# Performance work log

Measured on AMD Instinct MI355X. Metric: run time of the kernel, lower is better.

## Reference

```python
import jax, jax.numpy as jnp
import numpy as np


def lstm_cell(x, h, c, wih, whh, bih, bhh):
    # torch gate order: i, f, g, o
    g = x @ wih.T + bih + h @ whh.T + bhh
    i, f, gg, o = jnp.split(g, 4, axis=-1)
    c = jax.nn.sigmoid(f) * c + jax.nn.sigmoid(i) * jnp.tanh(gg)
    h = jax.nn.sigmoid(o) * jnp.tanh(c)
    return h, c


def lstm_layer(xs, h0, c0, wih, whh, bih, bhh):
    # xs: [T, B, in]
    def step(carry, x_t):
        h, c = lstm_cell(x_t, carry[0], carry[1], wih, whh, bih, bhh)
        return (h, c), h
    (h, c), hs = jax.lax.scan(step, (h0, c0), xs)
    return hs, h, c


def setup_inputs() -> dict:
    key = jax.random.key(0)
    B, T, H, IN = 256, 512, 512, 1
    ks = jax.random.split(key, 32)
    r = lambda k, shape: (jax.random.normal(k, shape, dtype=jnp.float32) * 0.05)
    inp = {
        "x": jax.random.normal(ks[0], (B, T, IN), dtype=jnp.float32),
        "future": 64,
        # main LSTM (2 layers)
        "w_ih0": r(ks[1], (4 * H, IN)), "w_hh0": r(ks[2], (4 * H, H)),
        "b_ih0": r(ks[3], (4 * H,)),   "b_hh0": r(ks[4], (4 * H,)),
        "w_ih1": r(ks[5], (4 * H, H)), "w_hh1": r(ks[6], (4 * H, H)),
        "b_ih1": r(ks[7], (4 * H,)),   "b_hh1": r(ks[8], (4 * H,)),
        "fc_w": r(ks[9], (1, H)),      "fc_b": r(ks[10], (1,)),
        # prediction LSTM (2 layers) + its head
        "pw_ih0": r(ks[11], (4 * H, 1)), "pw_hh0": r(ks[12], (4 * H, H)),
        "pb_ih0": r(ks[13], (4 * H,)),   "pb_hh0": r(ks[14], (4 * H,)),
        "pw_ih1": r(ks[15], (4 * H, H)), "pw_hh1": r(ks[16], (4 * H, H)),
        "pb_ih1": r(ks[17], (4 * H,)),   "pb_hh1": r(ks[18], (4 * H,)),
        "pfc_w": r(ks[19], (1, H)),      "pfc_b": r(ks[20], (1,)),
    }
    return inp


def reference(x, future, w_ih0, w_hh0, b_ih0, b_hh0, w_ih1, w_hh1, b_ih1, b_hh1,
              fc_w, fc_b, pw_ih0, pw_hh0, pb_ih0, pb_hh0, pw_ih1, pw_hh1,
              pb_ih1, pb_hh1, pfc_w, pfc_b):
    B = x.shape[0]
    H = w_hh0.shape[1]
    z = jnp.zeros((B, H), dtype=jnp.float32)
    xs = jnp.swapaxes(x, 0, 1)  # [T, B, 1]
    # warmup pass over the observed sequence (inference: dropout inactive)
    hs0, h0, c0 = lstm_layer(xs, z, z, w_ih0, w_hh0, b_ih0, b_hh0)
    hs1, h1, c1 = lstm_layer(hs0, z, z, w_ih1, w_hh1, b_ih1, b_hh1)
    out = hs1[-1] @ fc_w.T + fc_b  # [B, 1]

    def pstep(carry, _):
        o, h0, c0, h1, c1 = carry
        h0, c0 = lstm_cell(o, h0, c0, pw_ih0, pw_hh0, pb_ih0, pb_hh0)
        h1, c1 = lstm_cell(h0, h1, c1, pw_ih1, pw_hh1, pb_ih1, pb_hh1)
        o = h1 @ pfc_w.T + pfc_b
        return (o, h0, c0, h1, c1), o

    _, outs = jax.lax.scan(pstep, (out, h0, c0, h1, c1), None, length=future - 1)
    all_outs = jnp.concatenate([out[None], outs], axis=0)  # [future, B, 1]
    return jnp.swapaxes(all_outs[..., 0], 0, 1)  # [B, future]
```

## Files before the change

### kernel.cpp

```cpp
#include <hip/hip_runtime.h>
#include <hip/hip_bf16.h>

#define TT  512
#define BB  256
#define HH  512
#define FUT 64
#define NBLK 128


struct Hdr { int dtflag; };

typedef __attribute__((ext_vector_type(8))) short short8;
typedef __attribute__((ext_vector_type(4))) float floatx4;

#define OFF_FLG   4096
#define OFF_W     20480
#define WSZ       ((size_t)2048*512*2)
#define OFF_H0    (OFF_W + 6*WSZ)
#define HSZ       ((size_t)BB*HH*2)
#define OFF_H1    (OFF_H0 + 4*HSZ)
#define OFF_OA    (OFF_H1 + 2*HSZ)
#define OASZ      ((size_t)FUT*BB*4)
#define NEED_WS   (OFF_OA + OASZ)

#define SPIN_CAP  (1L << 22)

__device__ __forceinline__ float bf2f(short s) {
  unsigned u = ((unsigned)(unsigned short)s) << 16;
  return __builtin_bit_cast(float, u);
}
__device__ __forceinline__ short f2bf(float f) {
  unsigned u = __builtin_bit_cast(unsigned, f);
  u = u + 0x7FFFu + ((u >> 16) & 1u);
  return (short)(u >> 16);
}
__device__ __forceinline__ float ldf(const void* p, long i, int dt) {
  return dt ? ((const float*)p)[i] : bf2f(((const short*)p)[i]);
}
__device__ __forceinline__ short8 cohld16(const short* p) {
  short8 v;
  asm volatile("global_load_dwordx4 %0, %1, off sc0 sc1"
               : "=v"(v) : "v"(p));
  return v;
}
__device__ __forceinline__ void cohst16(short* p, short8 v) {
  asm volatile("global_store_dwordx4 %0, %1, off sc0 sc1"
               :: "v"(p), "v"(v) : "memory");
}
#define WAITV(N) do { asm volatile("s_waitcnt vmcnt(" #N ")" ::: "memory"); \
                      __builtin_amdgcn_sched_barrier(0); } while (0)

__global__ void beacon_kernel(float* dout, float v) {
  if (threadIdx.x == 0) dout[0] = v;
}

__global__ __launch_bounds__(256) void probe1_kernel(const void* w, Hdr* hdr) {
  const int tid = threadIdx.x;
  const short* s = (const short*)w;
  float mx = 0.f;
  #pragma unroll
  for (int i = 0; i < 16; ++i) {
    float v = fabsf(bf2f(s[tid * 16 + i]));
    if (!(v == v)) v = 1e30f;
    mx = fmaxf(mx, v);
  }
  #pragma unroll
  for (int off = 32; off > 0; off >>= 1) mx = fmaxf(mx, __shfl_down(mx, off));
  __shared__ float wmax[4];
  if ((tid & 63) == 0) wmax[tid >> 6] = mx;
  __syncthreads();
  if (tid == 0) {
    float m = fmaxf(fmaxf(wmax[0], wmax[1]), fmaxf(wmax[2], wmax[3]));
    hdr->dtflag = (m > 1000.f) ? 1 : 0;
  }
}

__global__ __launch_bounds__(256) void cvt_kernel(const void* src, short* dst,
                                                  const Hdr* hdr) {
  const int dt = hdr->dtflag;
  const long i = ((long)blockIdx.x * 256 + threadIdx.x);
  if (dt) {
    const float4 v = ((const float4*)src)[i];
    short4 o;
    o.x = f2bf(v.x); o.y = f2bf(v.y); o.z = f2bf(v.z); o.w = f2bf(v.w);
    ((short4*)dst)[i] = o;
  } else {
    ((short4*)dst)[i] = ((const short4*)src)[i];
  }
}

__global__ __launch_bounds__(512, 1) void lstm_persist(
    const void* __restrict__ x,
    const void* __restrict__ w_ih0, const void* __restrict__ b_ih0,
    const void* __restrict__ b_hh0, const void* __restrict__ b_ih1,
    const void* __restrict__ b_hh1, const void* __restrict__ fc_w,
    const void* __restrict__ fc_b,  const void* __restrict__ pw_ih0,
    const void* __restrict__ pb_ih0, const void* __restrict__ pb_hh0,
    const void* __restrict__ pb_ih1, const void* __restrict__ pb_hh1,
    const void* __restrict__ pfc_w, const void* __restrict__ pfc_b,
    const short* __restrict__ Whh0, const short* __restrict__ Wih1,
    const short* __restrict__ Whh1, const short* __restrict__ pWhh0,
    const short* __restrict__ pWih1, const short* __restrict__ pWhh1,
    short* H0R, short* H1R, float* oA, int* flg,
    const Hdr* __restrict__ hdr, float* __restrict__ dout)
{
  const int dt  = hdr->dtflag;
  const int tid = threadIdx.x;
  const int role = blockIdx.x & 1;
  const int bg   = (blockIdx.x >> 1) & 1;
  const int ug   = blockIdx.x >> 2;
  const int U0   = ug * 16;
  const int B0   = bg * 128;

  int* F     = flg + bg * 2048;
  int* pub0  = F;
  int* pub1  = F + 576;
  int* cons1 = F + 1152;
  int* opub  = F + 1728;

  __shared__ __align__(16) short Wl[2][64][64][8];
  __shared__ __align__(16) short hbuf[128][16];
  __shared__ float bs[64];
  __shared__ float wih[64];

  const int lane = tid & 63;
  const int wv   = tid >> 6;
  const int ln   = lane & 15;
  const int q    = lane >> 4;
  const int bl   = wv*16 + ln;
  const long abase = (long)(B0 + bl) * 512 + q*8;

  float cst[4] = {0.f, 0.f, 0.f, 0.f};
  float fwk[4] = {0.f, 0.f, 0.f, 0.f};

#define H0S(G) (H0R + (size_t)((G) & 3) * 131072)
#define H1S(G) (H1R + (size_t)((G) & 1) * 131072)

#define SPIN(COND)                                                           \
  { long guard_ = 0;                                                         \
    while (COND) {                                                           \
      __builtin_amdgcn_s_sleep(1);                                           \
      if (++guard_ > SPIN_CAP) break;                                        \
    } }
#define POLL(P, T)                                                           \
  SPIN(__hip_atomic_load((P), __ATOMIC_RELAXED,                              \
                         __HIP_MEMORY_SCOPE_SYSTEM) < (T))
#define FADD(P)                                                              \
  __hip_atomic_fetch_add((P), 1, __ATOMIC_RELAXED,                           \
                         __HIP_MEMORY_SCOPE_SYSTEM)

#define STAGE16(SLOT, WG)                                                    \
  for (int i = tid; i < 4096; i += 512) {                                    \
    const int ks_ = i & 63, r_ = i >> 6;                                     \
    const long gr = (long)((r_ & 3) * 512 + U0 + (r_ >> 2)) * 512 + ks_ * 8; \
    *(short8*)&Wl[SLOT][ks_][r_][0] = *(const short8*)((WG) + gr);           \
  }

#define BIAS16(B1, B2, WIHP)                                                 \
  if (tid < 64) {                                                            \
    const long j = (long)(tid & 3) * 512 + U0 + (tid >> 2);                  \
    bs[tid] = ldf((B1), j, dt) + ldf((B2), j, dt);                           \
    wih[tid] = (WIHP) ? ldf((const void*)(WIHP), j, dt) : 0.f;               \
  }

#define FWLOAD(FWP)                                                          \
  { _Pragma("unroll")                                                        \
    for (int mt = 0; mt < 4; ++mt)                                           \
      fwk[mt] = ldf((FWP), U0 + mt*4 + q, dt); }

#define ZACC(A)                                                              \
  _Pragma("unroll") for (int mt_ = 0; mt_ < 4; ++mt_)                        \
    A[mt_] = (floatx4){0.f, 0.f, 0.f, 0.f};

#define GSEG1N(AP, ACC)                                                      \
  { const short* ap_ = (AP) + abase;                                         \
    short8 abuf[2][8];                                                       \
    _Pragma("unroll")                                                        \
    for (int i = 0; i < 8; ++i) abuf[0][i] = cohld16(ap_ + i*32);            \
    _Pragma("unroll")                                                        \
    for (int g = 0; g < 2; ++g) {                                            \
      if (g == 0) {                                                          \
        _Pragma("unroll")                                                    \
        for (int i = 0; i < 8; ++i)                                          \
          abuf[1][i] = cohld16(ap_ + (8+i)*32);                              \
        WAITV(8);                                                            \
      } else { WAITV(0); }                                                   \
      _Pragma("unroll")                                                      \
      for (int kk = 0; kk < 8; ++kk) {                                       \
        const int kb = g*8 + kk;                                             \
        _Pragma("unroll")                                                    \
        for (int mt = 0; mt < 4; ++mt) {                                     \
          short8 wf = *(const short8*)&Wl[0][kb*4 + q][mt*16 + ln][0];       \
          ACC[mt] = __builtin_amdgcn_mfma_f32_16x16x32_bf16(                 \
              wf, abuf[g][kk], ACC[mt], 0, 0, 0);                            \
        }                                                                    \
      }                                                                      \
    } }

#define GSEG2N(AP0, AP1, ACC)                                                \
  { const short* p0_ = (AP0) + abase;                                        \
    const short* p1_ = (AP1) + abase;                                        \
    short8 abuf[2][8];                                                       \
    _Pragma("unroll")                                                        \
    for (int i = 0; i < 8; ++i) abuf[0][i] = cohld16(p0_ + i*32);            \
    _Pragma("unroll")                                                        \
    for (int g = 0; g < 4; ++g) {                                            \
      if (g < 3) {                                                           \
        const short* np_ = ((g+1)&1) ? p1_ : p0_;                            \
        const int nb_ = ((g+1)>>1)*8;                                        \
        _Pragma("unroll")                                                    \
        for (int i = 0; i < 8; ++i)                                          \
          abuf[(g+1)&1][i] = cohld16(np_ + (nb_+i)*32);                      \
        WAITV(8);                                                            \
      } else { WAITV(0); }                                                   \
      const int sg_ = g & 1;                                                 \
      const int kbb_ = (g >> 1) * 8;                                         \
      _Pragma("unroll")                                                      \
      for (int kk = 0; kk < 8; ++kk) {                                       \
        const int kb = kbb_ + kk;                                            \
        _Pragma("unroll")                                                    \
        for (int mt = 0; mt < 4; ++mt) {                                     \
          short8 wf = *(const short8*)&Wl[sg_][kb*4 + q][mt*16 + ln][0];     \
          ACC[mt] = __builtin_amdgcn_mfma_f32_16x16x32_bf16(                 \
              wf, abuf[g&1][kk], ACC[mt], 0, 0, 0);                          \
        }                                                                    \
      }                                                                      \
    } }

#define EPI16(ACC, MODE, TV, SVO, HOUT, OSLOT)                               \
  { float sv = 0.f;                                                          \
    if ((MODE) == 0)      sv = ldf(x, (long)(B0 + bl)*TT + (TV), dt);        \
    else if ((MODE) == 2) sv = (SVO);                                        \
    float po = 0.f;                                                          \
    _Pragma("unroll")                                                        \
    for (int mt = 0; mt < 4; ++mt) {                                         \
      const int u = mt*4 + q;                                                \
      float gi = ACC[mt][0] + bs[u*4+0];                                     \
      float gf = ACC[mt][1] + bs[u*4+1];                                     \
      float gg = ACC[mt][2] + bs[u*4+2];                                     \
      float go = ACC[mt][3] + bs[u*4+3];                                     \
      if ((MODE) != 1) {                                                     \
        gi += sv*wih[u*4+0]; gf += sv*wih[u*4+1];                            \
        gg += sv*wih[u*4+2]; go += sv*wih[u*4+3];                            \
      }                                                                      \
      const float I = 1.f/(1.f+expf(-gi));                                   \
      const float F = 1.f/(1.f+expf(-gf));                                   \
      const float G = tanhf(gg);                                             \
      const float O = 1.f/(1.f+expf(-go));                                   \
      const float cn = F*cst[mt] + I*G;                                      \
      cst[mt] = cn;                                                          \
      const short hb16 = f2bf(O * tanhf(cn));                                \
      hbuf[bl][u] = hb16;                                                    \
      if ((OSLOT) != (float*)0) po += fwk[mt] * bf2f(hb16);                  \
    }                                                                        \
    if ((OSLOT) != (float*)0) {                                              \
      po += __shfl_xor(po, 16); po += __shfl_xor(po, 32);                    \
      if (lane < 16) atomicAdd((float*)(OSLOT) + bl, po);                    \
    }                                                                        \
    __syncthreads();                                                         \
    if (tid < 256) {                                                         \
      const int b_ = tid >> 1, hf_ = tid & 1;                                \
      short8 hv8 = *(const short8*)&hbuf[b_][hf_*8];                         \
      cohst16((HOUT) + (long)(B0 + b_)*512 + U0 + hf_*8, hv8);               \
    }                                                                        \
    asm volatile("s_waitcnt vmcnt(0)" ::: "memory");                         \
    __syncthreads(); }

  if (role == 0) {
    STAGE16(0, Whh0);
    BIAS16(b_ih0, b_hh0, w_ih0);
  } else {
    STAGE16(0, Wih1); STAGE16(1, Whh1);
    BIAS16(b_ih1, b_hh1, (const void*)0);
    FWLOAD(fc_w);
  }
  const float fcb  = ldf(fc_b, 0, dt);
  const float pfcb = ldf(pfc_b, 0, dt);
  __syncthreads();

  if (role == 0) {
    for (int g = 0; g < TT; ++g) {
      if (tid == 0) {
        if (g > 0)  POLL(pub0 + g - 1, 32);
        if (g >= 4) POLL(cons1 + g - 4, 32);
      }
      __syncthreads();
      floatx4 a[4]; ZACC(a);
      GSEG1N(H0S(g-1), a);
      EPI16(a, 0, g, 0.f, H0S(g), (float*)0);
      if (tid == 0) FADD(pub0 + g);
    }
    STAGE16(0, pWhh0);
    BIAS16(pb_ih0, pb_hh0, pw_ih0);
    __syncthreads();
    for (int s = 1; s < FUT; ++s) {
      const int g = 511 + s;
      if (tid == 0) {
        POLL(pub0 + g - 1, 32);
        POLL(cons1 + g - 4, 32);
        POLL(opub + s - 1, 32);
      }
      __syncthreads();
      const float ob_ = (s == 1) ? fcb : pfcb;
      const float o_ = __hip_atomic_load(
          oA + (long)(s-1)*BB + B0 + bl,
          __ATOMIC_RELAXED, __HIP_MEMORY_SCOPE_SYSTEM) + ob_;
      if (ug == 0 && lane < 16)
        dout[(long)(B0 + bl)*FUT + (s-1)] = o_;
      floatx4 a[4]; ZACC(a);
      GSEG1N(H0S(g-1), a);
      EPI16(a, 2, 0, o_, H0S(g), (float*)0);
      if (tid == 0) FADD(pub0 + g);
    }
    if (tid == 0) POLL(opub + FUT - 1, 32);
    __syncthreads();
    if (ug == 0 && lane < 16) {
      const float o_ = __hip_atomic_load(
          oA + (long)(FUT-1)*BB + B0 + bl,
          __ATOMIC_RELAXED, __HIP_MEMORY_SCOPE_SYSTEM) + pfcb;
      dout[(long)(B0 + bl)*FUT + (FUT-1)] = o_;
    }
  } else {
    for (int g = 0; g < TT; ++g) {
      if (tid == 0) {
        POLL(pub0 + g, 32);
        if (g > 0) POLL(pub1 + g - 1, 32);
      }
      __syncthreads();
      floatx4 a[4]; ZACC(a);
      GSEG2N(H0S(g), H1S(g-1), a);
      __syncthreads();
      if (tid == 0) FADD(cons1 + g);
      float* os_ = (g == TT-1) ? (oA + B0) : (float*)0;
      EPI16(a, 1, 0, 0.f, H1S(g), os_);
      if (tid == 0) {
        FADD(pub1 + g);
        if (g == TT-1) FADD(opub + 0);
      }
    }
    STAGE16(0, pWih1); STAGE16(1, pWhh1);
    BIAS16(pb_ih1, pb_hh1, (const void*)0);
    FWLOAD(pfc_w);
    __syncthreads();
    for (int s = 1; s < FUT; ++s) {
      const int g = 511 + s;
      if (tid == 0) {
        POLL(pub0 + g, 32);
        POLL(pub1 + g - 1, 32);
      }
      __syncthreads();
      floatx4 a[4]; ZACC(a);
      GSEG2N(H0S(g), H1S(g-1), a);
      __syncthreads();
      if (tid == 0) FADD(cons1 + g);
      EPI16(a, 1, 0, 0.f, H1S(g), oA + (long)s*BB + B0);
      if (tid == 0) { FADD(pub1 + g); FADD(opub + s); }
    }
  }
#undef STAGE16
#undef BIAS16
#undef FWLOAD
#undef ZACC
#undef GSEG1N
#undef GSEG2N
#undef EPI16
#undef SPIN
#undef POLL
#undef FADD
#undef H0S
#undef H1S
}

extern "C" void kernel_launch(void* const* d_in, const int* in_sizes, int n_in,
                              void* d_out, int out_size, void* d_ws, size_t ws_size,
                              hipStream_t stream) {
  float* dout = (float*)d_out;

  static const int exp_sizes[22] = {
    131072, 1, 2048, 1048576, 2048, 2048, 1048576, 1048576, 2048, 2048,
    512, 1, 2048, 1048576, 2048, 2048, 1048576, 1048576, 2048, 2048, 512, 1};
  int code = -1, m = 0;
  if (n_in != 22) { code = 0; m = n_in & 127; }
  else {
    for (int i = 0; i < 22; ++i)
      if (in_sizes[i] != exp_sizes[i]) { code = 1; m = i; break; }
  }
  if (code < 0 && out_size != BB * FUT) { code = 6; m = (out_size >> 8) & 127; }
  if (code < 0 && (d_ws == nullptr || ws_size < NEED_WS)) {
    code = 2; m = (int)(ws_size >> 20); if (m > 127) m = 127;
  }
  if (code >= 0) {
    float v = ldexpf(1.f + (float)m / 128.f, 20 + code);
    beacon_kernel<<<dim3(1), dim3(64), 0, stream>>>(dout, v);
    return;
  }

  const void* x      = d_in[0];
  const void* w_ih0  = d_in[2];
  const void* w_hh0  = d_in[3];
  const void* b_ih0  = d_in[4];
  const void* b_hh0  = d_in[5];
  const void* w_ih1  = d_in[6];
  const void* w_hh1  = d_in[7];
  const void* b_ih1  = d_in[8];
  const void* b_hh1  = d_in[9];
  const void* fc_w   = d_in[10];
  const void* fc_b   = d_in[11];
  const void* pw_ih0 = d_in[12];
  const void* pw_hh0 = d_in[13];
  const void* pb_ih0 = d_in[14];
  const void* pb_hh0 = d_in[15];
  const void* pw_ih1 = d_in[16];
  const void* pw_hh1 = d_in[17];
  const void* pb_ih1 = d_in[18];
  const void* pb_hh1 = d_in[19];
  const void* pfc_w  = d_in[20];
  const void* pfc_b  = d_in[21];

  char* ws = (char*)d_ws;
  Hdr* hdr = (Hdr*)ws;
  int* flg = (int*)(ws + OFF_FLG);
  short* Wc[6];
  for (int i = 0; i < 6; ++i) Wc[i] = (short*)(ws + OFF_W + (size_t)i*WSZ);
  short* H0R = (short*)(ws + OFF_H0);
  short* H1R = (short*)(ws + OFF_H1);
  float* oA  = (float*)(ws + OFF_OA);

  hipMemsetAsync(ws, 0, 20480, stream);
  hipMemsetAsync(H0R, 0, 4*HSZ + 2*HSZ + OASZ, stream);
  probe1_kernel<<<dim3(1), dim3(256), 0, stream>>>(w_hh0, hdr);

  dim3 cg(1024), cb(256);
  cvt_kernel<<<cg, cb, 0, stream>>>(w_hh0,  Wc[0], hdr);
  cvt_kernel<<<cg, cb, 0, stream>>>(w_ih1,  Wc[1], hdr);
  cvt_kernel<<<cg, cb, 0, stream>>>(w_hh1,  Wc[2], hdr);
  cvt_kernel<<<cg, cb, 0, stream>>>(pw_hh0, Wc[3], hdr);
  cvt_kernel<<<cg, cb, 0, stream>>>(pw_ih1, Wc[4], hdr);
  cvt_kernel<<<cg, cb, 0, stream>>>(pw_hh1, Wc[5], hdr);

  lstm_persist<<<dim3(NBLK), dim3(512), 0, stream>>>(
      x, w_ih0, b_ih0, b_hh0, b_ih1, b_hh1, fc_w, fc_b,
      pw_ih0, pb_ih0, pb_hh0, pb_ih1, pb_hh1, pfc_w, pfc_b,
      Wc[0], Wc[1], Wc[2], Wc[3], Wc[4], Wc[5],
      H0R, H1R, oA, flg, hdr, dout);
}
```

Baseline: 6.714 ms.

## Partition persistent LSTM by XCC with per-group flags and local-coherence loads

Result: slower. 8.128 ms (+21.1%).

```diff
diff --git a/kernel.cpp b/kernel.cpp
--- a/kernel.cpp
+++ b/kernel.cpp
@@ -5,7 +5,7 @@
 #define BB  256
 #define HH  512
 #define FUT 64
-#define NBLK 128
+#define NBLK 256
 
 
 struct Hdr { int dtflag; };
@@ -13,17 +13,21 @@
 typedef __attribute__((ext_vector_type(8))) short short8;
 typedef __attribute__((ext_vector_type(4))) float floatx4;
 
-#define OFF_FLG   4096
-#define OFF_W     20480
-#define WSZ       ((size_t)2048*512*2)
-#define OFF_H0    (OFF_W + 6*WSZ)
-#define HSZ       ((size_t)BB*HH*2)
-#define OFF_H1    (OFF_H0 + 4*HSZ)
-#define OFF_OA    (OFF_H1 + 2*HSZ)
-#define OASZ      ((size_t)FUT*BB*4)
-#define NEED_WS   (OFF_OA + OASZ)
-
-#define SPIN_CAP  (1L << 22)
+#define OFF_XT   4096
+#define OFF_FLG  8192
+#define OFF_OP   12288
+#define OFF_PRB  98304
+#define OFF_H0   131072
+#define OFF_H1   (OFF_H0 + 524288)
+#define OFF_W    (OFF_H1 + 524288)
+#define WSZ      ((size_t)2048*512*2)
+#define NEED_WS  (OFF_W + 6*WSZ)
+
+#define SPIN_CAP  (1L << 18)
+#define RDV_CAP   (1L << 20)
+#define PROBE_CAP (1L << 15)
+#define MAG1 0x11C0FFEE
+#define MAG2 0x22C0FFEE
 
 __device__ __forceinline__ float bf2f(short s) {
   unsigned u = ((unsigned)(unsigned short)s) << 16;
@@ -37,13 +41,45 @@
 __device__ __forceinline__ float ldf(const void* p, long i, int dt) {
   return dt ? ((const float*)p)[i] : bf2f(((const short*)p)[i]);
 }
-__device__ __forceinline__ short8 cohld16(const short* p) {
-  short8 v;
-  asm volatile("global_load_dwordx4 %0, %1, off sc0 sc1"
+
+__device__ __forceinline__ int ld4s(const int* p) {
+  return __hip_atomic_load(p, __ATOMIC_RELAXED, __HIP_MEMORY_SCOPE_SYSTEM);
+}
+__device__ __forceinline__ void st4s(int* p, int v) {
+  __hip_atomic_store(p, v, __ATOMIC_RELAXED, __HIP_MEMORY_SCOPE_SYSTEM);
+}
+__device__ __forceinline__ void fadds(int* p) {
+  __hip_atomic_fetch_add(p, 1, __ATOMIC_RELAXED, __HIP_MEMORY_SCOPE_SYSTEM);
+}
+__device__ __forceinline__ int ld4l(const int* p) {
+  int v;
+  asm volatile("global_load_dword %0, %1, off sc0\n\ts_waitcnt vmcnt(0)"
                : "=v"(v) : "v"(p));
   return v;
 }
-__device__ __forceinline__ void cohst16(short* p, short8 v) {
+__device__ __forceinline__ void pollge(const int* p, int tgt, long cap) {
+  long g = 0;
+  while (ld4s(p) < tgt) {
+    __builtin_amdgcn_s_sleep(2);
+    if (++g > cap) break;
+  }
+}
+
+template<int IC>
+__device__ __forceinline__ short8 LDH(const short* p) {
+  short8 v;
+  if constexpr (IC)
+    asm volatile("global_load_dwordx4 %0, %1, off sc0 sc1" : "=v"(v) : "v"(p));
+  else
+    asm volatile("global_load_dwordx4 %0, %1, off sc0" : "=v"(v) : "v"(p));
+  return v;
+}
+__device__ __forceinline__ short8 LDW(const short* p) {
+  short8 v;
+  asm volatile("global_load_dwordx4 %0, %1, off" : "=v"(v) : "v"(p));
+  return v;
+}
+__device__ __forceinline__ void STH(short* p, short8 v) {
   asm volatile("global_store_dwordx4 %0, %1, off sc0 sc1"
                :: "v"(p), "v"(v) : "memory");
 }
@@ -89,6 +125,299 @@
   }
 }
 
+#define H0S(STEP) (h0ring + (size_t)(((STEP) & 1)) * 16384)
+#define H1S(STEP) (h1ring + (size_t)(((STEP) & 1)) * 16384)
+#define WLD(S, KB) \
+  (*(const short8*)(WlP + (((S)*64 + ((KB)*4 + q))*64 + (mt*16 + ln))*8))
+
+#define STAGE16(SLOT, WG)                                                    \
+  for (int i = tid; i < 4096; i += 512) {                                    \
+    const int ks_ = i & 63, r_ = i >> 6;                                     \
+    const long gr = (long)((r_ & 3)*512 + U0 + (r_ >> 2))*512 + ks_*8;       \
+    *(short8*)(WlP + (((SLOT)*64 + ks_)*64 + r_)*8) =                        \
+        *(const short8*)((WG) + gr);                                         \
+  }
+
+#define BIASLD(BA, B1, B2)                                                   \
+  if (tid < 64) {                                                            \
+    const long j_ = (long)(tid & 3)*512 + U0 + (tid >> 2);                   \
+    (BA)[tid] = ldf((B1), j_, dt) + ldf((B2), j_, dt);                       \
+  }
+#define WIHLD(WP)                                                            \
+  if (tid < 64) {                                                            \
+    const long j_ = (long)(tid & 3)*512 + U0 + (tid >> 2);                   \
+    wihL[tid] = ldf((WP), j_, dt);                                           \
+  }
+
+#define POLLF(TGT)                                                           \
+  { long gg_ = 0;                                                            \
+    for (;;) {                                                               \
+      int v_ = 0x7fffffff;                                                   \
+      if (lane < 32) v_ = ld4s(myflags + lane);                              \
+      if (__all(v_ >= (TGT))) break;                                         \
+      __builtin_amdgcn_s_sleep(2);                                           \
+      if (++gg_ > SPIN_CAP) break;                                           \
+    } }
+
+#define ZV ((floatx4){0.f, 0.f, 0.f, 0.f})
+
+#define GSEG_F(H0P, H1P, WSP)                                                \
+  { const short* hp0_ = (H0P) + hoff;                                        \
+    const short* hp1_ = (H1P) + hoff;                                        \
+    const short* wp_  = (WSP) + wrowoff;                                     \
+    short8 bw[2][4], c0b[2][4], c1b[2][4];                                   \
+    _Pragma("unroll")                                                        \
+    for (int i = 0; i < 4; ++i) {                                            \
+      bw[0][i]  = LDW(wp_ + i*32);                                           \
+      c0b[0][i] = LDH<IC>(hp0_ + i*32);                                      \
+      c1b[0][i] = LDH<IC>(hp1_ + i*32);                                      \
+    }                                                                        \
+    _Pragma("unroll")                                                        \
+    for (int g = 0; g < 4; ++g) {                                            \
+      if (g < 3) {                                                           \
+        _Pragma("unroll")                                                    \
+        for (int i = 0; i < 4; ++i) {                                        \
+          const int kb_ = (g+1)*4 + i;                                       \
+          bw[(g+1)&1][i]  = LDW(wp_ + kb_*32);                               \
+          c0b[(g+1)&1][i] = LDH<IC>(hp0_ + kb_*32);                          \
+          c1b[(g+1)&1][i] = LDH<IC>(hp1_ + kb_*32);                          \
+        }                                                                    \
+        WAITV(12);                                                           \
+      } else { WAITV(0); }                                                   \
+      _Pragma("unroll")                                                      \
+      for (int i = 0; i < 4; ++i) {                                          \
+        const int kb_ = g*4 + i;                                             \
+        a0 = __builtin_amdgcn_mfma_f32_16x16x32_bf16(                        \
+            bw[g&1][i], c0b[g&1][i], a0, 0, 0, 0);                           \
+        a1 = __builtin_amdgcn_mfma_f32_16x16x32_bf16(                        \
+            WLD(0, kb_), c0b[g&1][i], a1, 0, 0, 0);                          \
+        a1 = __builtin_amdgcn_mfma_f32_16x16x32_bf16(                        \
+            WLD(1, kb_), c1b[g&1][i], a1, 0, 0, 0);                          \
+      }                                                                      \
+    } }
+
+#define GSEG_A(H0P, WSP)                                                     \
+  { const short* hp0_ = (H0P) + hoff;                                        \
+    const short* wp_  = (WSP) + wrowoff;                                     \
+    short8 bw[2][4], c0b[2][4];                                              \
+    _Pragma("unroll")                                                        \
+    for (int i = 0; i < 4; ++i) {                                            \
+      bw[0][i]  = LDW(wp_ + i*32);                                           \
+      c0b[0][i] = LDH<IC>(hp0_ + i*32);                                      \
+    }                                                                        \
+    _Pragma("unroll")                                                        \
+    for (int g = 0; g < 4; ++g) {                                            \
+      if (g < 3) {                                                           \
+        _Pragma("unroll")                                                    \
+        for (int i = 0; i < 4; ++i) {                                        \
+          const int kb_ = (g+1)*4 + i;                                       \
+          bw[(g+1)&1][i]  = LDW(wp_ + kb_*32);                               \
+          c0b[(g+1)&1][i] = LDH<IC>(hp0_ + kb_*32);                          \
+        }                                                                    \
+        WAITV(8);                                                            \
+      } else { WAITV(0); }                                                   \
+      _Pragma("unroll")                                                      \
+      for (int i = 0; i < 4; ++i)                                            \
+        a0 = __builtin_amdgcn_mfma_f32_16x16x32_bf16(                        \
+            bw[g&1][i], c0b[g&1][i], a0, 0, 0, 0);                           \
+    } }
+
+#define GSEG_B(H0P, H1P)                                                     \
+  { const short* hp0_ = (H0P) + hoff;                                        \
+    const short* hp1_ = (H1P) + hoff;                                        \
+    short8 c0b[2][4], c1b[2][4];                                             \
+    _Pragma("unroll")                                                        \
+    for (int i = 0; i < 4; ++i) {                                            \
+      c0b[0][i] = LDH<IC>(hp0_ + i*32);                                      \
+      c1b[0][i] = LDH<IC>(hp1_ + i*32);                                      \
+    }                                                                        \
+    _Pragma("unroll")                                                        \
+    for (int g = 0; g < 4; ++g) {                                            \
+      if (g < 3) {                                                           \
+        _Pragma("unroll")                                                    \
+        for (int i = 0; i < 4; ++i) {                                        \
+          const int kb_ = (g+1)*4 + i;                                       \
+          c0b[(g+1)&1][i] = LDH<IC>(hp0_ + kb_*32);                          \
+          c1b[(g+1)&1][i] = LDH<IC>(hp1_ + kb_*32);                          \
+        }                                                                    \
+        WAITV(8);                                                            \
+      } else { WAITV(0); }                                                   \
+      _Pragma("unroll")                                                      \
+      for (int i = 0; i < 4; ++i) {                                          \
+        const int kb_ = g*4 + i;                                             \
+        a1 = __builtin_amdgcn_mfma_f32_16x16x32_bf16(                        \
+            WLD(0, kb_), c0b[g&1][i], a1, 0, 0, 0);                          \
+        a1 = __builtin_amdgcn_mfma_f32_16x16x32_bf16(                        \
+            WLD(1, kb_), c1b[g&1][i], a1, 0, 0, 0);                          \
+      }                                                                      \
+    } }
+
+#define EPIX(D0, D1, MODE, HEAD, PAR, H0ST, H1ST, TVAL)                      \
+  { float sv_ = 0.f;                                                         \
+    if ((MODE) == 0)      sv_ = ldf(x, (long)(B0 + b)*TT + (TVAL), dt);      \
+    else if ((MODE) == 2) sv_ = obuf[b];                                     \
+    if (D0) {                                                                \
+      float gi = a0[0] + bsA[u*4+0] + sv_*wihL[u*4+0];                       \
+      float gf = a0[1] + bsA[u*4+1] + sv_*wihL[u*4+1];                       \
+      float gg = a0[2] + bsA[u*4+2] + sv_*wihL[u*4+2];                       \
+      float go = a0[3] + bsA[u*4+3] + sv_*wihL[u*4+3];                       \
+      const float I = 1.f/(1.f+expf(-gi));                                   \
+      const float F = 1.f/(1.f+expf(-gf));                                   \
+      const float G = tanhf(gg);                                             \
+      const float O = 1.f/(1.f+expf(-go));                                   \
+      cst0 = F*cst0 + I*G;                                                   \
+      hb0[b*16 + u] = f2bf(O * tanhf(cst0));                                 \
+    }                                                                        \
+    if (D1) {                                                                \
+      float gi = a1[0] + bsB[u*4+0];                                         \
+      float gf = a1[1] + bsB[u*4+1];                                         \
+      float gg = a1[2] + bsB[u*4+2];                                         \
+      float go = a1[3] + bsB[u*4+3];                                         \
+      const float I = 1.f/(1.f+expf(-gi));                                   \
+      const float F = 1.f/(1.f+expf(-gf));                                   \
+      const float G = tanhf(gg);                                             \
+      const float O = 1.f/(1.f+expf(-go));                                   \
+      cst1 = F*cst1 + I*G;                                                   \
+      const float hv_ = O * tanhf(cst1);                                     \
+      hb1[b*16 + u] = f2bf(hv_);                                             \
+      if (HEAD) {                                                            \
+        float po_ = fw * hv_;                                                \
+        po_ += __shfl_xor(po_, 16);                                          \
+        po_ += __shfl_xor(po_, 32);                                          \
+        if (lane < 16) opl[mt*32 + b] = po_;                                 \
+      }                                                                      \
+    }                                                                        \
+    __syncthreads();                                                         \
+    if ((D0) && tid < 64)                                                    \
+      STH(H0S(H0ST) + (long)(tid>>1)*512 + U0 + (tid&1)*8,                   \
+          *(const short8*)(hb0 + (tid>>1)*16 + (tid&1)*8));                  \
+    if ((D1) && tid >= 64 && tid < 128) {                                    \
+      const int t_ = tid - 64;                                               \
+      STH(H1S(H1ST) + (long)(t_>>1)*512 + U0 + (t_&1)*8,                     \
+          *(const short8*)(hb1 + (t_>>1)*16 + (t_&1)*8));                    \
+    }                                                                        \
+    if ((HEAD) && tid < 32) {                                                \
+      union { float f; int i; } uo_;                                         \
+      uo_.f = opl[tid] + opl[32+tid] + opl[64+tid] + opl[96+tid];            \
+      st4s((int*)(opb + (PAR)*1024 + tid*32 + ug), uo_.i);                   \
+    }                                                                        \
+    asm volatile("s_waitcnt vmcnt(0)" ::: "memory");                         \
+    __syncthreads();                                                         \
+  }
+
+#define PUBF(V) do { if (tid == 0) st4s(myflags + ug, (V)); } while (0)
+
+#define OBUFC(PAR, OBIAS, OUTCOL)                                            \
+  if (tid < 32) {                                                            \
+    const float* pp_ = opb + (PAR)*1024 + tid*32;                            \
+    short8 r_[8];                                                            \
+    _Pragma("unroll")                                                        \
+    for (int j = 0; j < 8; ++j)                                              \
+      r_[j] = LDH<IC>((const short*)(pp_ + j*4));                            \
+    WAITV(0);                                                                \
+    float s_ = 0.f;                                                          \
+    _Pragma("unroll")                                                        \
+    for (int j = 0; j < 8; ++j) {                                            \
+      union { short8 v; float f[4]; } cv_; cv_.v = r_[j];                    \
+      s_ += cv_.f[0] + cv_.f[1] + cv_.f[2] + cv_.f[3];                       \
+    }                                                                        \
+    const float o_ = s_ + (OBIAS);                                           \
+    obuf[tid] = o_;                                                          \
+    if (ug == 0) dout[(long)(B0 + tid)*FUT + (OUTCOL)] = o_;                 \
+  }
+
+template<int IC>
+__device__ __forceinline__ void lstm_run(
+    int dt, int bg, int ug, int tid,
+    const void* x, const void* w_ih0, const void* b_ih0, const void* b_hh0,
+    const void* b_ih1, const void* b_hh1, const void* fc_w, const void* fc_b,
+    const void* pw_ih0, const void* pb_ih0, const void* pb_hh0,
+    const void* pb_ih1, const void* pb_hh1, const void* pfc_w,
+    const void* pfc_b,
+    const short* Whh0c, const short* Wih1c, const short* Whh1c,
+    const short* pWhh0c, const short* pWih1c, const short* pWhh1c,
+    short* h0ring, short* h1ring, float* opb, int* myflags,
+    float* dout,
+    short* WlP, short* hb0, short* hb1,
+    float* bsA, float* bsB, float* wihL, float* obuf, float* opl)
+{
+  const int lane = tid & 63, wv = tid >> 6;
+  const int ln = lane & 15, q = lane >> 4;
+  const int mt = wv >> 1, bt = wv & 1;
+  const int u  = mt*4 + q;
+  const int b  = bt*16 + ln;
+  const int U0 = ug * 16;
+  const int B0 = bg * 32;
+  const long hoff = (long)b*512 + q*8;
+  const int  Rr = mt*16 + ln;
+  const long wrowoff = ((long)(Rr & 3)*512 + U0 + (Rr >> 2))*512 + q*8;
+
+  float cst0 = 0.f, cst1 = 0.f;
+  float fw = ldf(fc_w, U0 + u, dt);
+  const float fcb  = ldf(fc_b, 0, dt);
+  const float pfcb = ldf(pfc_b, 0, dt);
+
+  STAGE16(0, Wih1c); STAGE16(1, Whh1c);
+  BIASLD(bsA, b_ih0, b_hh0); BIASLD(bsB, b_ih1, b_hh1); WIHLD(w_ih0);
+  __syncthreads();
+
+  floatx4 a0, a1;
+  int p = 0;
+  for (int t = 0; t < TT; ++t, ++p) {
+    POLLF(p);
+    a0 = ZV; a1 = ZV;
+    if (t == 0) {
+      GSEG_A(H0S(-1), Whh0c);
+      EPIX(1, 0, 0, 0, 0, 0, 0, t);
+    } else {
+      GSEG_F(H0S(t-1), H1S(t-2), Whh0c);
+      EPIX(1, 1, 0, 0, 0, t, t-1, t);
+    }
+    PUBF(p + 1);
+  }
+  {
+    POLLF(p);
+    a1 = ZV;
+    GSEG_B(H0S(511), H1S(510));
+    EPIX(0, 1, 1, 1, 0, 0, 511, 0);
+    PUBF(p + 1); ++p;
+  }
+  STAGE16(0, pWih1c); STAGE16(1, pWhh1c);
+  BIASLD(bsA, pb_ih0, pb_hh0); BIASLD(bsB, pb_ih1, pb_hh1); WIHLD(pw_ih0);
+  fw = ldf(pfc_w, U0 + u, dt);
+  __syncthreads();
+  for (int s = 1; s < FUT; ++s) {
+    POLLF(p);
+    OBUFC((s-1) & 1, (s == 1) ? fcb : pfcb, s-1);
+    a0 = ZV;
+    GSEG_A(H0S(510 + s), pWhh0c);
+    __syncthreads();
+    EPIX(1, 0, 2, 0, 0, 511 + s, 0, 0);
+    PUBF(p + 1); ++p;
+
+    POLLF(p);
+    a1 = ZV;
+    GSEG_B(H0S(511 + s), H1S(510 + s));
+    EPIX(0, 1, 1, 1, s & 1, 0, 511 + s, 0);
+    PUBF(p + 1); ++p;
+  }
+  POLLF(p);
+  if (ug == 0 && tid < 32) {
+    const float* pp = opb + ((FUT-1) & 1)*1024 + tid*32;
+    short8 r[8];
+    #pragma unroll
+    for (int j = 0; j < 8; ++j) r[j] = LDH<IC>((const short*)(pp + j*4));
+    WAITV(0);
+    float s = 0.f;
+    #pragma unroll
+    for (int j = 0; j < 8; ++j) {
+      union { short8 v; float f[4]; } cv; cv.v = r[j];
+      s += cv.f[0] + cv.f[1] + cv.f[2] + cv.f[3];
+    }
+    dout[(long)(B0 + tid)*FUT + (FUT-1)] = s + pfcb;
+  }
+}
+
 __global__ __launch_bounds__(512, 1) void lstm_persist(
     const void* __restrict__ x,
     const void* __restrict__ w_ih0, const void* __restrict__ b_ih0,
@@ -98,277 +427,131 @@
     const void* __restrict__ pb_ih0, const void* __restrict__ pb_hh0,
     const void* __restrict__ pb_ih1, const void* __restrict__ pb_hh1,
     const void* __restrict__ pfc_w, const void* __restrict__ pfc_b,
-    const short* __restrict__ Whh0, const short* __restrict__ Wih1,
-    const short* __restrict__ Whh1, const short* __restrict__ pWhh0,
-    const short* __restrict__ pWih1, const short* __restrict__ pWhh1,
-    short* H0R, short* H1R, float* oA, int* flg,
+    const short* __restrict__ Whh0c, const short* __restrict__ Wih1c,
+    const short* __restrict__ Whh1c, const short* __restrict__ pWhh0c,
+    const short* __restrict__ pWih1c, const short* __restrict__ pWhh1c,
+    short* H0R, short* H1R, float* oA, int* xt, int* flg, int* prb,
     const Hdr* __restrict__ hdr, float* __restrict__ dout)
 {
+  __shared__ __align__(16) short Wl[2*64*64*8];
+  __shared__ __align__(16) short hb0[512], hb1[512];
+  __shared__ float bsA[64], bsB[64], wihL[64], obuf[32], opl[128];
+  __shared__ int xls[256];
+  __shared__ int meta[4];
+
+  const int tid = threadIdx.x;
+  const int bid = blockIdx.x;
   const int dt  = hdr->dtflag;
-  const int tid = threadIdx.x;
-  const int role = blockIdx.x & 1;
-  const int bg   = (blockIdx.x >> 1) & 1;
-  const int ug   = blockIdx.x >> 2;
-  const int U0   = ug * 16;
-  const int B0   = bg * 128;
-
-  int* F     = flg + bg * 2048;
-  int* pub0  = F;
-  int* pub1  = F + 576;
-  int* cons1 = F + 1152;
-  int* opub  = F + 1728;
-
-  __shared__ __align__(16) short Wl[2][64][64][8];
-  __shared__ __align__(16) short hbuf[128][16];
-  __shared__ float bs[64];
-  __shared__ float wih[64];
-
-  const int lane = tid & 63;
-  const int wv   = tid >> 6;
-  const int ln   = lane & 15;
-  const int q    = lane >> 4;
-  const int bl   = wv*16 + ln;
-  const long abase = (long)(B0 + bl) * 512 + q*8;
-
-  float cst[4] = {0.f, 0.f, 0.f, 0.f};
-  float fwk[4] = {0.f, 0.f, 0.f, 0.f};
-
-#define H0S(G) (H0R + (size_t)((G) & 3) * 131072)
-#define H1S(G) (H1R + (size_t)((G) & 1) * 131072)
-
-#define SPIN(COND)                                                           \
-  { long guard_ = 0;                                                         \
-    while (COND) {                                                           \
-      __builtin_amdgcn_s_sleep(1);                                           \
-      if (++guard_ > SPIN_CAP) break;                                        \
-    } }
-#define POLL(P, T)                                                           \
-  SPIN(__hip_atomic_load((P), __ATOMIC_RELAXED,                              \
-                         __HIP_MEMORY_SCOPE_SYSTEM) < (T))
-#define FADD(P)                                                              \
-  __hip_atomic_fetch_add((P), 1, __ATOMIC_RELAXED,                           \
-                         __HIP_MEMORY_SCOPE_SYSTEM)
-
-#define STAGE16(SLOT, WG)                                                    \
-  for (int i = tid; i < 4096; i += 512) {                                    \
-    const int ks_ = i & 63, r_ = i >> 6;                                     \
-    const long gr = (long)((r_ & 3) * 512 + U0 + (r_ >> 2)) * 512 + ks_ * 8; \
-    *(short8*)&Wl[SLOT][ks_][r_][0] = *(const short8*)((WG) + gr);           \
-  }
-
-#define BIAS16(B1, B2, WIHP)                                                 \
-  if (tid < 64) {                                                            \
-    const long j = (long)(tid & 3) * 512 + U0 + (tid >> 2);                  \
-    bs[tid] = ldf((B1), j, dt) + ldf((B2), j, dt);                           \
-    wih[tid] = (WIHP) ? ldf((const void*)(WIHP), j, dt) : 0.f;               \
-  }
-
-#define FWLOAD(FWP)                                                          \
-  { _Pragma("unroll")                                                        \
-    for (int mt = 0; mt < 4; ++mt)                                           \
-      fwk[mt] = ldf((FWP), U0 + mt*4 + q, dt); }
-
-#define ZACC(A)                                                              \
-  _Pragma("unroll") for (int mt_ = 0; mt_ < 4; ++mt_)                        \
-    A[mt_] = (floatx4){0.f, 0.f, 0.f, 0.f};
-
-#define GSEG1N(AP, ACC)                                                      \
-  { const short* ap_ = (AP) + abase;                                         \
-    short8 abuf[2][8];                                                       \
-    _Pragma("unroll")                                                        \
-    for (int i = 0; i < 8; ++i) abuf[0][i] = cohld16(ap_ + i*32);            \
-    _Pragma("unroll")                                                        \
-    for (int g = 0; g < 2; ++g) {                                            \
-      if (g == 0) {                                                          \
-        _Pragma("unroll")                                                    \
-        for (int i = 0; i < 8; ++i)                                          \
-          abuf[1][i] = cohld16(ap_ + (8+i)*32);                              \
-        WAITV(8);                                                            \
-      } else { WAITV(0); }                                                   \
-      _Pragma("unroll")                                                      \
-      for (int kk = 0; kk < 8; ++kk) {                                       \
-        const int kb = g*8 + kk;                                             \
-        _Pragma("unroll")                                                    \
-        for (int mt = 0; mt < 4; ++mt) {                                     \
-          short8 wf = *(const short8*)&Wl[0][kb*4 + q][mt*16 + ln][0];       \
-          ACC[mt] = __builtin_amdgcn_mfma_f32_16x16x32_bf16(                 \
-              wf, abuf[g][kk], ACC[mt], 0, 0, 0);                            \
-        }                                                                    \
-      }                                                                      \
-    } }
-
-#define GSEG2N(AP0, AP1, ACC)                                                \
-  { const short* p0_ = (AP0) + abase;                                        \
-    const short* p1_ = (AP1) + abase;                                        \
-    short8 abuf[2][8];                                                       \
-    _Pragma("unroll")                                                        \
-    for (int i = 0; i < 8; ++i) abuf[0][i] = cohld16(p0_ + i*32);            \
-    _Pragma("unroll")                                                        \
-    for (int g = 0; g < 4; ++g) {                                            \
-      if (g < 3) {                                                           \
-        const short* np_ = ((g+1)&1) ? p1_ : p0_;                            \
-        const int nb_ = ((g+1)>>1)*8;                                        \
-        _Pragma("unroll")                                                    \
-        for (int i = 0; i < 8; ++i)                                          \
-          abuf[(g+1)&1][i] = cohld16(np_ + (nb_+i)*32);                      \
-        WAITV(8);                                                            \
-      } else { WAITV(0); }                                                   \
-      const int sg_ = g & 1;                                                 \
-      const int kbb_ = (g >> 1) * 8;                                         \
-      _Pragma("unroll")                                                      \
-      for (int kk = 0; kk < 8; ++kk) {                                       \
-        const int kb = kbb_ + kk;                                            \
-        _Pragma("unroll")                                                    \
-        for (int mt = 0; mt < 4; ++mt) {                                     \
-          short8 wf = *(const short8*)&Wl[sg_][kb*4 + q][mt*16 + ln][0];     \
-          ACC[mt] = __builtin_amdgcn_mfma_f32_16x16x32_bf16(                 \
-              wf, abuf[g&1][kk], ACC[mt], 0, 0, 0);                          \
-        }                                                                    \
-      }                                                                      \
-    } }
-
-#define EPI16(ACC, MODE, TV, SVO, HOUT, OSLOT)                               \
-  { float sv = 0.f;                                                          \
-    if ((MODE) == 0)      sv = ldf(x, (long)(B0 + bl)*TT + (TV), dt);        \
-    else if ((MODE) == 2) sv = (SVO);                                        \
-    float po = 0.f;                                                          \
-    _Pragma("unroll")                                                        \
-    for (int mt = 0; mt < 4; ++mt) {                                         \
-      const int u = mt*4 + q;                                                \
-      float gi = ACC[mt][0] + bs[u*4+0];                                     \
-      float gf = ACC[mt][1] + bs[u*4+1];                                     \
-      float gg = ACC[mt][2] + bs[u*4+2];                                     \
-      float go = ACC[mt][3] + bs[u*4+3];                                     \
-      if ((MODE) != 1) {                                                     \
-        gi += sv*wih[u*4+0]; gf += sv*wih[u*4+1];                            \
-        gg += sv*wih[u*4+2]; go += sv*wih[u*4+3];                            \
-      }                                                                      \
-      const float I = 1.f/(1.f+expf(-gi));                                   \
-      const float F = 1.f/(1.f+expf(-gf));                                   \
-      const float G = tanhf(gg);                                             \
-      const float O = 1.f/(1.f+expf(-go));                                   \
-      const float cn = F*cst[mt] + I*G;                                      \
-      cst[mt] = cn;                                                          \
-      const short hb16 = f2bf(O * tanhf(cn));                                \
-      hbuf[bl][u] = hb16;                                                    \
-      if ((OSLOT) != (float*)0) po += fwk[mt] * bf2f(hb16);                  \
-    }                                                                        \
-    if ((OSLOT) != (float*)0) {                                              \
-      po += __shfl_xor(po, 16); po += __shfl_xor(po, 32);                    \
-      if (lane < 16) atomicAdd((float*)(OSLOT) + bl, po);                    \
-    }                                                                        \
-    __syncthreads();                                                         \
-    if (tid < 256) {                                                         \
-      const int b_ = tid >> 1, hf_ = tid & 1;                                \
-      short8 hv8 = *(const short8*)&hbuf[b_][hf_*8];                         \
-      cohst16((HOUT) + (long)(B0 + b_)*512 + U0 + hf_*8, hv8);               \
-    }                                                                        \
-    asm volatile("s_waitcnt vmcnt(0)" ::: "memory");                         \
-    __syncthreads(); }
-
-  if (role == 0) {
-    STAGE16(0, Whh0);
-    BIAS16(b_ih0, b_hh0, w_ih0);
-  } else {
-    STAGE16(0, Wih1); STAGE16(1, Whh1);
-    BIAS16(b_ih1, b_hh1, (const void*)0);
-    FWLOAD(fc_w);
-  }
-  const float fcb  = ldf(fc_b, 0, dt);
-  const float pfcb = ldf(pfc_b, 0, dt);
+
+  if (tid == 0) {
+    int xcc = 0;
+    asm volatile("s_getreg_b32 %0, hwreg(HW_REG_XCC_ID)" : "=s"(xcc));
+    __hip_atomic_store(xt + bid, (xcc & 7) + 1, __ATOMIC_RELAXED,
+                       __HIP_MEMORY_SCOPE_SYSTEM);
+  }
+  if (tid < 64) {
+    long gg = 0;
+    for (;;) {
+      int ok = 1;
+      #pragma unroll
+      for (int j = 0; j < 4; ++j) {
+        int v = ld4s(xt + tid*4 + j);
+        xls[tid*4 + j] = v;
+        ok &= (v != 0);
+      }
+      if (__all(ok)) break;
+      __builtin_amdgcn_s_sleep(2);
+      if (++gg > RDV_CAP) break;
+    }
+  }
   __syncthreads();
-
-  if (role == 0) {
-    for (int g = 0; g < TT; ++g) {
-      if (tid == 0) {
-        if (g > 0)  POLL(pub0 + g - 1, 32);
-        if (g >= 4) POLL(cons1 + g - 4, 32);
-      }
-      __syncthreads();
-      floatx4 a[4]; ZACC(a);
-      GSEG1N(H0S(g-1), a);
-      EPI16(a, 0, g, 0.f, H0S(g), (float*)0);
-      if (tid == 0) FADD(pub0 + g);
-    }
-    STAGE16(0, pWhh0);
-    BIAS16(pb_ih0, pb_hh0, pw_ih0);
-    __syncthreads();
-    for (int s = 1; s < FUT; ++s) {
-      const int g = 511 + s;
-      if (tid == 0) {
-        POLL(pub0 + g - 1, 32);
-        POLL(cons1 + g - 4, 32);
-        POLL(opub + s - 1, 32);
-      }
-      __syncthreads();
-      const float ob_ = (s == 1) ? fcb : pfcb;
-      const float o_ = __hip_atomic_load(
-          oA + (long)(s-1)*BB + B0 + bl,
-          __ATOMIC_RELAXED, __HIP_MEMORY_SCOPE_SYSTEM) + ob_;
-      if (ug == 0 && lane < 16)
-        dout[(long)(B0 + bl)*FUT + (s-1)] = o_;
-      floatx4 a[4]; ZACC(a);
-      GSEG1N(H0S(g-1), a);
-      EPI16(a, 2, 0, o_, H0S(g), (float*)0);
-      if (tid == 0) FADD(pub0 + g);
-    }
-    if (tid == 0) POLL(opub + FUT - 1, 32);
-    __syncthreads();
-    if (ug == 0 && lane < 16) {
-      const float o_ = __hip_atomic_load(
-          oA + (long)(FUT-1)*BB + B0 + bl,
-          __ATOMIC_RELAXED, __HIP_MEMORY_SCOPE_SYSTEM) + pfcb;
-      dout[(long)(B0 + bl)*FUT + (FUT-1)] = o_;
-    }
-  } else {
-    for (int g = 0; g < TT; ++g) {
-      if (tid == 0) {
-        POLL(pub0 + g, 32);
-        if (g > 0) POLL(pub1 + g - 1, 32);
-      }
-      __syncthreads();
-      floatx4 a[4]; ZACC(a);
-      GSEG2N(H0S(g), H1S(g-1), a);
-      __syncthreads();
-      if (tid == 0) FADD(cons1 + g);
-      float* os_ = (g == TT-1) ? (oA + B0) : (float*)0;
-      EPI16(a, 1, 0, 0.f, H1S(g), os_);
-      if (tid == 0) {
-        FADD(pub1 + g);
-        if (g == TT-1) FADD(opub + 0);
+  if (tid == 0) {
+    int total[8] = {0,0,0,0,0,0,0,0};
+    for (int i = 0; i < NBLK; ++i) total[(xls[i] - 1) & 7]++;
+    int cnt[8] = {0,0,0,0,0,0,0,0};
+    int mybg = -1, myug = -1, nover = 0, orank = -1;
+    for (int i = 0; i < NBLK; ++i) {
+      const int xi = (xls[i] - 1) & 7;
+      if (cnt[xi] < 32) {
+        if (i == bid) { mybg = xi; myug = cnt[xi]; }
+        cnt[xi]++;
+      } else {
+        if (i == bid) orank = nover;
+        nover++;
       }
     }
-    STAGE16(0, pWih1); STAGE16(1, pWhh1);
-    BIAS16(pb_ih1, pb_hh1, (const void*)0);
-    FWLOAD(pfc_w);
-    __syncthreads();
-    for (int s = 1; s < FUT; ++s) {
-      const int g = 511 + s;
-      if (tid == 0) {
-        POLL(pub0 + g, 32);
-        POLL(pub1 + g - 1, 32);
+    if (mybg < 0) {
+      int d = 0;
+      for (int k = 0; k < 8 && mybg < 0; ++k) {
+        const int miss = 32 - cnt[k];
+        if (miss > 0) {
+          if (orank < d + miss) { mybg = k; myug = cnt[k] + (orank - d); }
+          d += miss;
+        }
       }
-      __syncthreads();
-      floatx4 a[4]; ZACC(a);
-      GSEG2N(H0S(g), H1S(g-1), a);
-      __syncthreads();
-      if (tid == 0) FADD(cons1 + g);
-      EPI16(a, 1, 0, 0.f, H1S(g), oA + (long)s*BB + B0);
-      if (tid == 0) { FADD(pub1 + g); FADD(opub + s); }
     }
-  }
-#undef STAGE16
-#undef BIAS16
-#undef FWLOAD
-#undef ZACC
-#undef GSEG1N
-#undef GSEG2N
-#undef EPI16
-#undef SPIN
-#undef POLL
-#undef FADD
-#undef H0S
-#undef H1S
+    int loc;
+    if (mybg < 0 || myug < 0 || myug > 31) {
+      mybg = bid >> 5; myug = bid & 31; loc = 0;
+    } else {
+      loc = (total[mybg] >= 32) ? 1 : 0;
+    }
+    meta[0] = mybg; meta[1] = myug; meta[2] = loc;
+  }
+  __syncthreads();
+  const int bg = meta[0], ug = meta[1], loc = meta[2];
+
+  int dec = 0;
+  if (tid == 0 && loc) {
+    int* pb = prb + bg * 64;
+    if (ug == 0) {
+      pollge(pb + 4, 31, PROBE_CAP);
+      st4s(pb, MAG1);
+      asm volatile("s_waitcnt vmcnt(0)" ::: "memory");
+      st4s(pb + 5, 1);
+      pollge(pb + 6, 31, PROBE_CAP);
+      st4s(pb, MAG2);
+      asm volatile("s_waitcnt vmcnt(0)" ::: "memory");
+      st4s(pb + 7, 1);
+      pollge(pb + 9, 31, PROBE_CAP);
+      const int d = (ld4s(pb + 8) == 31) ? 2 : 1;
+      st4s(pb + 10, d);
+      dec = (d == 2);
+    } else {
+      (void)ld4l(pb);
+      fadds(pb + 4);
+      pollge(pb + 5, 1, PROBE_CAP);
+      int ok = (ld4l(pb) == MAG1);
+      fadds(pb + 6);
+      pollge(pb + 7, 1, PROBE_CAP);
+      ok = ok && (ld4l(pb) == MAG2);
+      if (ok) fadds(pb + 8);
+      fadds(pb + 9);
+      pollge(pb + 10, 1, PROBE_CAP);
+      dec = (ld4s(pb + 10) == 2);
+    }
+  }
+  if (tid == 0) meta[3] = dec;
+  __syncthreads();
+  const int uselocal = meta[3];
+
+  short* h0ring  = H0R + (size_t)bg * 32768;
+  short* h1ring  = H1R + (size_t)bg * 32768;
+  float* opb     = oA + (size_t)bg * 2048;
+  int*   myflags = flg + bg * 32;
+
+  if (uselocal)
+    lstm_run<0>(dt, bg, ug, tid, x, w_ih0, b_ih0, b_hh0, b_ih1, b_hh1,
+                fc_w, fc_b, pw_ih0, pb_ih0, pb_hh0, pb_ih1, pb_hh1,
+                pfc_w, pfc_b, Whh0c, Wih1c, Whh1c, pWhh0c, pWih1c, pWhh1c,
+                h0ring, h1ring, opb, myflags, dout,
+                Wl, hb0, hb1, bsA, bsB, wihL, obuf, opl);
+  else
+    lstm_run<1>(dt, bg, ug, tid, x, w_ih0, b_ih0, b_hh0, b_ih1, b_hh1,
+                fc_w, fc_b, pw_ih0, pb_ih0, pb_hh0, pb_ih1, pb_hh1,
+                pfc_w, pfc_b, Whh0c, Wih1c, Whh1c, pWhh0c, pWih1c, pWhh1c,
+                h0ring, h1ring, opb, myflags, dout,
+                Wl, hb0, hb1, bsA, bsB, wihL, obuf, opl);
 }
 
 extern "C" void kernel_launch(void* const* d_in, const int* in_sizes, int n_in,
@@ -419,15 +602,17 @@
 
   char* ws = (char*)d_ws;
   Hdr* hdr = (Hdr*)ws;
+  int* xt  = (int*)(ws + OFF_XT);
   int* flg = (int*)(ws + OFF_FLG);
+  float* oA = (float*)(ws + OFF_OP);
+  int* prb = (int*)(ws + OFF_PRB);
+  short* H0R = (short*)(ws + OFF_H0);
+  short* H1R = (short*)(ws + OFF_H1);
   short* Wc[6];
   for (int i = 0; i < 6; ++i) Wc[i] = (short*)(ws + OFF_W + (size_t)i*WSZ);
-  short* H0R = (short*)(ws + OFF_H0);
-  short* H1R = (short*)(ws + OFF_H1);
-  float* oA  = (float*)(ws + OFF_OA);
-
-  hipMemsetAsync(ws, 0, 20480, stream);
-  hipMemsetAsync(H0R, 0, 4*HSZ + 2*HSZ + OASZ, stream);
+
+  hipMemsetAsync(ws, 0, OFF_H0, stream);
+  hipMemsetAsync(ws + OFF_H0, 0, 1048576, stream);
   probe1_kernel<<<dim3(1), dim3(256), 0, stream>>>(w_hh0, hdr);
 
   dim3 cg(1024), cb(256);
@@ -442,5 +627,5 @@
       x, w_ih0, b_ih0, b_hh0, b_ih1, b_hh1, fc_w, fc_b,
       pw_ih0, pb_ih0, pb_hh0, pb_ih1, pb_hh1, pfc_w, pfc_b,
       Wc[0], Wc[1], Wc[2], Wc[3], Wc[4], Wc[5],
-      H0R, H1R, oA, flg, hdr, dout);
-}
+      H0R, H1R, oA, xt, flg, prb, hdr, dout);
+}
```
